# Performance work log

Hardware: AMD Instinct MI355X
Metric: run time of the kernel (lower is better)

## Reference

```python
import jax, jax.numpy as jnp
import numpy as np

WS = 8          # window_size
NH = 8          # num_heads
IQKV = 128      # inner_qk_v_dim
IQKC = 32       # inner_qk_c_dim
IVV = 64        # inner_v_v_dim
EPS = 1e-6
B, HH, WW, DV, DC = 2, 224, 224, 256, 64


def _rmsnorm(x, g):
    return x * jax.lax.rsqrt(jnp.mean(x * x, axis=-1, keepdims=True) + EPS) * g


def _window(x):
    # (b, h, w, d) -> (b, Wh, Ww, ws*ws, d)
    b, h, w, d = x.shape
    x = x.reshape(b, h // WS, WS, w // WS, WS, d).transpose(0, 1, 3, 2, 4, 5)
    return x.reshape(b, h // WS, w // WS, WS * WS, d)


def _unwindow(x, h, w):
    # (b, N, ws*ws, d) -> (b, h, w, d)
    b, _, _, d = x.shape
    x = x.reshape(b, h // WS, w // WS, WS, WS, d).transpose(0, 1, 3, 2, 4, 5)
    return x.reshape(b, h, w, d)


def _source_qkv(V, C, Wqk_v, bqk_v, g_v, Wqk_c, bqk_c, g_c, Wv):
    Vw, Cw = _window(V), _window(C)          # (b, Wh, Ww, n, d)
    b, Wh, Ww, n, _ = Vw.shape
    N = Wh * Ww
    Vavg, Cavg = Vw.mean(-2), Cw.mean(-2)
    qk_v = _rmsnorm(Vavg @ Wqk_v + bqk_v, g_v)   # (b, Wh, Ww, 2*IQKV)
    qk_c = _rmsnorm(Cavg @ Wqk_c + bqk_c, g_c)   # (b, Wh, Ww, 2*IQKC)
    # 'b Wh Ww (H e) -> b H (Wh Ww) e' then chunk2 along e
    qk_v = qk_v.reshape(b, N, NH, -1).transpose(0, 2, 1, 3)
    qk_c = qk_c.reshape(b, N, NH, -1).transpose(0, 2, 1, 3)
    ev, ec = qk_v.shape[-1] // 2, qk_c.shape[-1] // 2
    qv, kv = qk_v[..., :ev], qk_v[..., ev:]
    qc, kc = qk_c[..., :ec], qk_c[..., ec:]
    # value projection: 'b Wh Ww n (e H) -> b H (Wh Ww) (n e)'
    e = IVV // NH
    Vv = (Vw @ Wv).reshape(b, N, n, e, NH).transpose(0, 4, 1, 2, 3).reshape(b, NH, N, n * e)
    return qv, kv, qc, kc, Vv, (Wh, Ww)


def _forward(values0, coords0, values1, coords1,
             Wqk_v, bqk_v, g_v, Wqk_c, bqk_c, g_c, Wv, Wback):
    parts = [_source_qkv(V, C, Wqk_v, bqk_v, g_v, Wqk_c, bqk_c, g_c, Wv)
             for V, C in ((values0, coords0), (values1, coords1))]
    qv = jnp.concatenate([p[0] for p in parts], axis=2)
    kv = jnp.concatenate([p[1] for p in parts], axis=2)
    qc = jnp.concatenate([p[2] for p in parts], axis=2)
    kc = jnp.concatenate([p[3] for p in parts], axis=2)
    Vv = jnp.concatenate([p[4] for p in parts], axis=2)
    scores = (jnp.einsum('bhqe,bhke->bhqk', qv, kv) / jnp.sqrt(jnp.float32(IQKV))
              + jnp.einsum('bhqe,bhke->bhqk', qc, kc) / jnp.sqrt(jnp.float32(IQKC)))
    A = jax.nn.softmax(scores, axis=-1)            # (b, H, N, N)
    rw = jnp.einsum('bhqk,bhkf->bhqf', A, Vv)      # (b, H, N, n*e)
    b, _, N, _ = rw.shape
    n, e = WS * WS, IVV // NH
    # 'b H N (n e) -> b N n (e H)'
    rw = rw.reshape(b, NH, N, n, e).transpose(0, 2, 3, 4, 1).reshape(b, N, n, e * NH)
    rw = rw @ Wback                                # (b, N, n, Dv)
    outs, off = [], 0
    for (V, _), p in zip(((values0, coords0), (values1, coords1)), parts):
        Wh, Ww = p[5]
        Ns = Wh * Ww
        outs.append(_unwindow(rw[:, off:off + Ns], Wh * WS, Ww * WS))
        off += Ns
    return tuple(outs)


def setup_inputs() -> dict:
    key = jax.random.key(0)
    ks = jax.random.split(key, 8)
    s = 0.02
    return {
        'values0': jax.random.normal(ks[0], (B, HH, WW, DV), jnp.float32),
        'coords0': jax.random.normal(ks[1], (B, HH, WW, DC), jnp.float32),
        'values1': jax.random.normal(ks[2], (B, HH, WW, DV), jnp.float32),
        'coords1': jax.random.normal(ks[3], (B, HH, WW, DC), jnp.float32),
        'Wqk_v': s * jax.random.normal(ks[4], (DV, 2 * IQKV), jnp.float32),
        'bqk_v': jnp.zeros((2 * IQKV,), jnp.float32),
        'g_v': jnp.ones((2 * IQKV,), jnp.float32),
        'Wqk_c': s * jax.random.normal(ks[5], (DC, 2 * IQKC), jnp.float32),
        'bqk_c': jnp.zeros((2 * IQKC,), jnp.float32),
        'g_c': jnp.ones((2 * IQKC,), jnp.float32),
        'Wv': s * jax.random.normal(ks[6], (DV, IVV), jnp.float32),
        'Wback': s * jax.random.normal(ks[7], (IVV, DV), jnp.float32),
    }


def reference(values0, coords0, values1, coords1,
              Wqk_v, bqk_v, g_v, Wqk_c, bqk_c, g_c, Wv, Wback):
    return _forward(values0, coords0, values1, coords1,
                    Wqk_v, bqk_v, g_v, Wqk_c, bqk_c, g_c, Wv, Wback)
```

## Files before the change

kernel.cpp:

```cpp
#include <hip/hip_runtime.h>

#define NSRC 784
#define NTOT 1568
#define NHD 8
#define DVC 256
#define DCC 64
#define D20 20
#define FDIM 512
#define OUT_PER_SRC 25690112

typedef short s16x8 __attribute__((ext_vector_type(8)));
typedef unsigned short u16x8 __attribute__((ext_vector_type(8)));
typedef unsigned short u16x4 __attribute__((ext_vector_type(4)));
typedef float f32x4 __attribute__((ext_vector_type(4)));
typedef float f32x16 __attribute__((ext_vector_type(16)));
typedef unsigned u32x4 __attribute__((ext_vector_type(4)));

__device__ __forceinline__ unsigned short f2bf(float x) {
    unsigned u = __float_as_uint(x);
    unsigned r = (u + 0x7FFFu + ((u >> 16) & 1u)) >> 16;
    return (unsigned short)r;
}

__device__ __forceinline__ unsigned cvt_pk_bf16(float lo, float hi) {
    unsigned r;
    asm volatile("v_cvt_pk_bf16_f32 %0, %1, %2" : "=v"(r) : "v"(lo), "v"(hi));
    return r;
}

__device__ __forceinline__ void split_bf(float x, unsigned short& hi, unsigned short& lo) {
    unsigned short h = f2bf(x);
    float hf = __uint_as_float(((unsigned)h) << 16);
    hi = h;
    lo = f2bf(x - hf);
}

__global__ __launch_bounds__(256) void kz_zero(unsigned short* __restrict__ p) {
    size_t i = (size_t)blockIdx.x * 256 + threadIdx.x;
    u16x8 z = (u16x8)0;
    *(u16x8*)&p[i * 8] = z;
}

__global__ __launch_bounds__(256) void k0_wsplit(
    const float* __restrict__ Wv,
    unsigned short* __restrict__ WThi, unsigned short* __restrict__ WTlo) {
    int e = blockIdx.x, dd = threadIdx.x;
    float x = Wv[dd * DCC + e];
    unsigned short h, l;
    split_bf(x, h, l);
    WThi[e * 256 + dd] = h;
    WTlo[e * 256 + dd] = l;
}

__global__ __launch_bounds__(256) void k0b_wback(
    const float* __restrict__ Wb, unsigned short* __restrict__ Wp) {
    int idx = blockIdx.x * 256 + threadIdx.x;
    int jj = idx & 7, lane = (idx >> 3) & 63, hl = (idx >> 9) & 1;
    int kc = (idx >> 10) & 1, mt = idx >> 11;
    int c = mt * 16 + (lane & 15);
    int j = kc * 32 + (lane >> 4) * 8 + jj;
    unsigned short h, l;
    split_bf(Wb[j * 256 + c], h, l);
    Wp[idx] = hl ? l : h;
}

__global__ __launch_bounds__(256) void k1c_avg(
    const float* __restrict__ c0, const float* __restrict__ c1,
    float* __restrict__ Cavg) {
    int wi = blockIdx.x * 4 + (threadIdx.x >> 6);
    int d = threadIdx.x & 63;
    int b = wi / NTOT, N = wi % NTOT;
    int src = N / NSRC, nloc = N % NSRC;
    int wh = nloc / 28, ww = nloc % 28;
    const float* __restrict__ C = src ? c1 : c0;
    int pbase = (b * 224 + wh * 8) * 224 + ww * 8;
    float s = 0.f;
#pragma unroll 8
    for (int p = 0; p < 64; ++p)
        s += C[(size_t)(pbase + (p >> 3) * 224 + (p & 7)) * DCC + d];
    Cavg[(size_t)wi * DCC + d] = s * 0.015625f;
}

__global__ __launch_bounds__(256) void k2_qk(
    const float* __restrict__ Vavg, const float* __restrict__ Cavg,
    const float* __restrict__ Wqkv, const float* __restrict__ bqkv, const float* __restrict__ gv,
    const float* __restrict__ Wqkc, const float* __restrict__ bqkc, const float* __restrict__ gc,
    unsigned short* __restrict__ Qp, unsigned short* __restrict__ Kp) {
    __shared__ float xv[DVC];
    __shared__ float xc[DCC];
    __shared__ float wred[4];
    int blk = blockIdx.x;
    int b = blk / NTOT, N = blk % NTOT;
    int t = threadIdx.x;
    int tile = N >> 5, l31 = N & 31;
    xv[t] = Vavg[(size_t)blk * DVC + t];
    if (t < DCC) xc[t] = Cavg[(size_t)blk * DCC + t];
    __syncthreads();
    float yv = bqkv[t];
#pragma unroll 4
    for (int d = 0; d < DVC; ++d) yv += xv[d] * Wqkv[d * 256 + t];
    float ss = yv * yv;
#pragma unroll
    for (int off = 32; off; off >>= 1) ss += __shfl_xor(ss, off, 64);
    if ((t & 63) == 0) wred[t >> 6] = ss;
    __syncthreads();
    float tot = wred[0] + wred[1] + wred[2] + wred[3];
    float rv = rsqrtf(tot * (1.f / 256.f) + 1e-6f);
    float yn = yv * rv * gv[t];
    int h = t >> 5, c = t & 31;
    int bh = b * NHD + h;
    {
        int isq = (c < 16);
        int d = isq ? c : c - 16;
        float val = isq ? yn * 0.088388347648318447f : yn;
        unsigned short h16, l16;
        split_bf(val, h16, l16);
        int hh = d >> 3, j = d & 7;
        size_t base = ((size_t)(bh * 49 + tile) * 4) * 512 + (size_t)(hh * 32 + l31) * 8 + j;
        unsigned short* dst = isq ? Qp : Kp;
        dst[base] = h16;
        dst[base + 1024] = l16;
    }
    if (t < DCC) {
        float yc = bqkc[t];
#pragma unroll 4
        for (int d = 0; d < DCC; ++d) yc += xc[d] * Wqkc[d * 64 + t];
        float sc = yc * yc;
#pragma unroll
        for (int off = 32; off; off >>= 1) sc += __shfl_xor(sc, off, 64);
        float rc = rsqrtf(sc * (1.f / 64.f) + 1e-6f);
        float ycn = yc * rc * gc[t];
        int h2 = t >> 3, c2 = t & 7;
        int bh2 = b * NHD + h2;
        int isq = (c2 < 4);
        int dd = isq ? c2 : c2 - 4;
        float val = isq ? ycn * 0.17677669529663687f : ycn;
        unsigned short h16, l16;
        split_bf(val, h16, l16);
        size_t base = ((size_t)(bh2 * 49 + tile) * 4 + 1) * 512 + (size_t)l31 * 8 + dd;
        unsigned short* dst = isq ? Qp : Kp;
        dst[base] = h16;
        dst[base + 1024] = l16;
    }
}

__global__ __launch_bounds__(256) void k3_vv(
    const float* __restrict__ v0, const float* __restrict__ v1,
    const unsigned short* __restrict__ WThi, const unsigned short* __restrict__ WTlo,
    unsigned short* __restrict__ Vvb, float* __restrict__ Vavg) {
    __shared__ unsigned short Ahi[64 * 138];
    __shared__ unsigned short Alo[64 * 138];
    int blk = blockIdx.x;
    int b = blk / NTOT, N = blk % NTOT;
    int src = N / NSRC, nloc = N % NSRC;
    int wh = nloc / 28, ww = nloc % 28;
    const float* __restrict__ V = src ? v1 : v0;
    int t = threadIdx.x;
    int w = t >> 6, lane = t & 63;
    int lm = lane & 15, lk = lane >> 4;
    int pxw = w * 16;
    int lhalf = lane >> 5;
    int d4 = (lane & 31) * 4;
    int pbase = (b * 224 + wh * 8) * 224 + ww * 8;

    float ap[8] = {0.f, 0.f, 0.f, 0.f, 0.f, 0.f, 0.f, 0.f};
    f32x4 acc4[4];
#pragma unroll
    for (int nt = 0; nt < 4; ++nt) acc4[nt] = (f32x4)0.f;

#pragma unroll
    for (int ph = 0; ph < 2; ++ph) {
        int d0 = ph * 128;
        float4 xs[8];
#pragma unroll
        for (int i = 0; i < 8; ++i) {
            int px = pxw + i * 2 + lhalf;
            xs[i] = *(const float4*)&V[(size_t)(pbase + (px >> 3) * 224 + (px & 7)) * DVC + d0 + d4];
        }
#pragma unroll
        for (int i = 0; i < 8; ++i) {
            ap[ph * 4 + 0] += xs[i].x; ap[ph * 4 + 1] += xs[i].y;
            ap[ph * 4 + 2] += xs[i].z; ap[ph * 4 + 3] += xs[i].w;
        }
        if (ph) __syncthreads();
#pragma unroll
        for (int i = 0; i < 8; ++i) {
            int px = pxw + i * 2 + lhalf;
            u16x4 h4, l4;
            unsigned short hq, lq;
            split_bf(xs[i].x, hq, lq); h4[0] = hq; l4[0] = lq;
            split_bf(xs[i].y, hq, lq); h4[1] = hq; l4[1] = lq;
            split_bf(xs[i].z, hq, lq); h4[2] = hq; l4[2] = lq;
            split_bf(xs[i].w, hq, lq); h4[3] = hq; l4[3] = lq;
            *(u16x4*)&Ahi[px * 138 + d4] = h4;
            *(u16x4*)&Alo[px * 138 + d4] = l4;
        }
        __syncthreads();
#pragma unroll
        for (int c2 = 0; c2 < 4; ++c2) {
            int dd0 = c2 * 32;
            s16x8 ahi = *(const s16x8*)&Ahi[(pxw + lm) * 138 + dd0 + lk * 8];
            s16x8 alo = *(const s16x8*)&Alo[(pxw + lm) * 138 + dd0 + lk * 8];
#pragma unroll
            for (int nt = 0; nt < 4; ++nt) {
                int e = nt * 16 + lm;
                s16x8 bhi = *(const s16x8*)&WThi[e * 256 + d0 + dd0 + lk * 8];
                s16x8 blo = *(const s16x8*)&WTlo[e * 256 + d0 + dd0 + lk * 8];
                acc4[nt] = __builtin_amdgcn_mfma_f32_16x16x32_bf16(ahi, blo, acc4[nt], 0, 0, 0);
                acc4[nt] = __builtin_amdgcn_mfma_f32_16x16x32_bf16(alo, bhi, acc4[nt], 0, 0, 0);
                acc4[nt] = __builtin_amdgcn_mfma_f32_16x16x32_bf16(ahi, bhi, acc4[nt], 0, 0, 0);
            }
        }
    }
#pragma unroll
    for (int nt = 0; nt < 4; ++nt) {
        int e = nt * 16 + lm;
#pragma unroll
        for (int r = 0; r < 4; ++r) {
            int px = w * 16 + lk * 4 + r;
            Vvb[((size_t)(b * NHD + (e & 7)) * NTOT + N) * FDIM + px * 8 + (e >> 3)] = f2bf(acc4[nt][r]);
        }
    }
#pragma unroll
    for (int j = 0; j < 8; ++j) ap[j] += __shfl_xor(ap[j], 32, 64);
    __syncthreads();
    float* avgb = (float*)Ahi;
    if (lhalf == 0) {
#pragma unroll
        for (int ph = 0; ph < 2; ++ph) {
            float4 v4 = make_float4(ap[ph * 4], ap[ph * 4 + 1], ap[ph * 4 + 2], ap[ph * 4 + 3]);
            *(float4*)&avgb[w * 256 + ph * 128 + d4] = v4;
        }
    }
    __syncthreads();
    Vavg[(size_t)blk * DVC + t] =
        (avgb[t] + avgb[256 + t] + avgb[512 + t] + avgb[768 + t]) * 0.015625f;
}

__global__ __launch_bounds__(256) void k3b_pack(
    const unsigned short* __restrict__ Vvb, unsigned short* __restrict__ Vp) {
    __shared__ unsigned short tile[32 * 520];
    int kt = blockIdx.x, bh = blockIdx.y;
    int t = threadIdx.x;
    const unsigned short* src = Vvb + ((size_t)bh * NTOT + kt * 32) * FDIM;
#pragma unroll
    for (int it = 0; it < 8; ++it) {
        int flat = it * 256 + t;
        int r = flat >> 6, c8 = (flat & 63) * 8;
        *(u16x8*)&tile[r * 520 + c8] = *(const u16x8*)&src[(size_t)r * FDIM + c8];
    }
    __syncthreads();
    unsigned short* dst = Vp + ((size_t)bh * 49 + kt) * 16384;
#pragma unroll
    for (int it = 0; it < 8; ++it) {
        int flato = it * 256 + t;
        int lane = flato & 63;
        int kh = (flato >> 6) & 1;
        int sub = (flato >> 7) & 3;
        int w = flato >> 9;
        int l31 = lane & 31, hh = lane >> 5;
        int f = w * 128 + sub * 32 + l31;
        int kbase = kh * 16 + hh * 8;
        u16x8 v;
#pragma unroll
        for (int j = 0; j < 8; ++j) v[j] = tile[(kbase + j) * 520 + f];
        *(u16x8*)&dst[(size_t)flato * 8] = v;
    }
}

__global__ __launch_bounds__(256) void k4_attn(
    const unsigned short* __restrict__ Qp, const unsigned short* __restrict__ Kp,
    const unsigned short* __restrict__ Vp, float* __restrict__ rw) {
    __shared__ float ebuf[32 * 132];
    int wg = blockIdx.x;
    int qt = wg >> 4, bh = wg & 15;
    int q0 = qt * 32;
    int t = threadIdx.x;
    int w = t >> 6, lane = t & 63;
    int l31 = lane & 31, hh = lane >> 5;

    const unsigned short* __restrict__ Qpb = Qp + ((size_t)(bh * 49 + qt) * 4) * 512 + lane * 8;
    const unsigned short* __restrict__ Kpb = Kp + (size_t)bh * 49 * 2048 + lane * 8;
    const unsigned short* __restrict__ Vpb = Vp + (size_t)bh * 49 * 16384 + lane * 8;

    s16x8 qa0 = *(const s16x8*)&Qpb[0];
    s16x8 qa1 = *(const s16x8*)&Qpb[512];
    s16x8 ql0 = *(const s16x8*)&Qpb[1024];
    s16x8 ql1 = *(const s16x8*)&Qpb[1536];

    s16x8 ka0 = *(const s16x8*)&Kpb[0];
    s16x8 ka1 = *(const s16x8*)&Kpb[512];
    s16x8 kl0 = *(const s16x8*)&Kpb[1024];
    s16x8 kl1 = *(const s16x8*)&Kpb[1536];

    float m = -1e30f, lsum = 0.f;
    f32x16 acc[4];
#pragma unroll
    for (int s = 0; s < 4; ++s) acc[s] = (f32x16)0.f;

    for (int kt = 0; kt < NTOT / 32; ++kt) {
        const unsigned short* Vtile = Vpb + (size_t)kt * 16384 + (w * 8) * 512;
        s16x8 va[8];
#pragma unroll
        for (int fr = 0; fr < 8; ++fr)
            va[fr] = *(const s16x8*)&Vtile[fr * 512];
        int ktn = (kt < 48) ? kt + 1 : 48;
        const unsigned short* Ktn = Kpb + (size_t)ktn * 2048;
        s16x8 kn0 = *(const s16x8*)&Ktn[0];
        s16x8 kn1 = *(const s16x8*)&Ktn[512];
        s16x8 kn2 = *(const s16x8*)&Ktn[1024];
        s16x8 kn3 = *(const s16x8*)&Ktn[1536];

        f32x16 sacc = (f32x16)0.f;
        sacc = __builtin_amdgcn_mfma_f32_32x32x16_bf16(kl0, qa0, sacc, 0, 0, 0);
        sacc = __builtin_amdgcn_mfma_f32_32x32x16_bf16(ka0, ql0, sacc, 0, 0, 0);
        sacc = __builtin_amdgcn_mfma_f32_32x32x16_bf16(ka0, qa0, sacc, 0, 0, 0);
        sacc = __builtin_amdgcn_mfma_f32_32x32x16_bf16(kl1, qa1, sacc, 0, 0, 0);
        sacc = __builtin_amdgcn_mfma_f32_32x32x16_bf16(ka1, ql1, sacc, 0, 0, 0);
        sacc = __builtin_amdgcn_mfma_f32_32x32x16_bf16(ka1, qa1, sacc, 0, 0, 0);

        float tmax = sacc[0];
#pragma unroll
        for (int r = 1; r < 16; ++r) tmax = fmaxf(tmax, sacc[r]);
        tmax = fmaxf(tmax, __shfl_xor(tmax, 32, 64));
        if (__any(tmax > m + 8.f)) {
            float mn = fmaxf(m, tmax);
            float sc = __expf(m - mn);
#pragma unroll
            for (int s = 0; s < 4; ++s) acc[s] = acc[s] * sc;
            lsum *= sc;
            m = mn;
        }
        unsigned P2[8];
        float tsum = 0.f;
#pragma unroll
        for (int j = 0; j < 8; ++j) {
            float pa = __expf(sacc[2 * j] - m);
            float pb = __expf(sacc[2 * j + 1] - m);
            tsum += pa + pb;
            P2[j] = cvt_pk_bf16(pa, pb);
        }
        lsum += tsum + __shfl_xor(tsum, 32, 64);
        unsigned X2[8];
#pragma unroll
        for (int j = 0; j < 8; ++j) X2[j] = (unsigned)__shfl_xor((int)P2[j], 32, 64);
        u32x4 b0u, b1u;
        if (hh == 0) {
            b0u[0] = P2[0]; b0u[1] = P2[1]; b0u[2] = X2[0]; b0u[3] = X2[1];
            b1u[0] = P2[4]; b1u[1] = P2[5]; b1u[2] = X2[4]; b1u[3] = X2[5];
        } else {
            b0u[0] = X2[2]; b0u[1] = X2[3]; b0u[2] = P2[2]; b0u[3] = P2[3];
            b1u[0] = X2[6]; b1u[1] = X2[7]; b1u[2] = P2[6]; b1u[3] = P2[7];
        }
        s16x8 pb0 = __builtin_bit_cast(s16x8, b0u);
        s16x8 pb1 = __builtin_bit_cast(s16x8, b1u);

#pragma unroll
        for (int sub = 0; sub < 4; ++sub) {
            acc[sub] = __builtin_amdgcn_mfma_f32_32x32x16_bf16(va[2 * sub],     pb0, acc[sub], 0, 0, 0);
            acc[sub] = __builtin_amdgcn_mfma_f32_32x32x16_bf16(va[2 * sub + 1], pb1, acc[sub], 0, 0, 0);
        }
        ka0 = kn0; ka1 = kn1; kl0 = kn2; kl1 = kn3;
    }

    float inv = 1.f / lsum;
    float* rwg = rw + ((size_t)bh * NTOT + q0) * FDIM;
#pragma unroll
    for (int c = 0; c < 4; ++c) {
        __syncthreads();
        if (w == c) {
#pragma unroll
            for (int sub = 0; sub < 4; ++sub) {
#pragma unroll
                for (int r = 0; r < 16; ++r) {
                    int fl = sub * 32 + (r & 3) + 8 * (r >> 2) + 4 * hh;
                    ebuf[l31 * 132 + fl] = acc[sub][r] * inv;
                }
            }
        }
        __syncthreads();
        int qr = t >> 3, cb = (t & 7) * 16;
#pragma unroll
        for (int j = 0; j < 4; ++j) {
            *(float4*)&rwg[(size_t)qr * FDIM + c * 128 + cb + j * 4] =
                *(const float4*)&ebuf[qr * 132 + cb + j * 4];
        }
    }
}

__global__ __launch_bounds__(256) void k5_back(
    const float* __restrict__ rw, const unsigned short* __restrict__ Wp,
    float* __restrict__ out) {
    __shared__ unsigned short SB[2 * 64 * 72];
    unsigned short* BhL = SB;
    unsigned short* BlL = SB + 64 * 72;
    int blk = blockIdx.x;
    int b = blk / NTOT, N = blk % NTOT;
    int src = N / NSRC, nloc = N % NSRC;
    int wh = nloc / 28, ww = nloc % 28;
    int t = threadIdx.x;
    int w = t >> 6, lane = t & 63;
    int lm = lane & 15, lk = lane >> 4;
    int pbase = (b * 224 + wh * 8) * 224 + ww * 8;

#pragma unroll
    for (int i = 0; i < 4; ++i) {
        int flat4 = i * 256 + t;
        int h = flat4 >> 7;
        int f0 = (flat4 & 127) * 4;
        float4 v = *(const float4*)&rw[((size_t)(b * NHD + h) * NTOT + N) * FDIM + f0];
        int n = f0 >> 3;
        int ebase = f0 & 7;
        float vv[4] = {v.x, v.y, v.z, v.w};
#pragma unroll
        for (int u = 0; u < 4; ++u) {
            int j8 = ebase + u;
            unsigned short h16, l16;
            split_bf(vv[u], h16, l16);
            int col = ((j8 ^ (n & 7)) << 3) | h;
            BhL[n * 72 + col] = h16;
            BlL[n * 72 + col] = l16;
        }
    }
    __syncthreads();

    f32x4 acc[4][4];
#pragma unroll
    for (int mi = 0; mi < 4; ++mi)
#pragma unroll
        for (int nt = 0; nt < 4; ++nt) acc[mi][nt] = (f32x4)0.f;

    const unsigned short* Wpw = Wp + (size_t)(w * 4) * 2048 + lane * 8;
#pragma unroll
    for (int kc = 0; kc < 2; ++kc) {
        s16x8 Ah[4], Al[4], Bh4[4], Bl4[4];
#pragma unroll
        for (int mi = 0; mi < 4; ++mi) {
            int base = mi * 2048 + kc * 1024;
            Ah[mi] = *(const s16x8*)&Wpw[base];
            Al[mi] = *(const s16x8*)&Wpw[base + 512];
        }
#pragma unroll
        for (int nt = 0; nt < 4; ++nt) {
            int n = nt * 16 + lm;
            int addr = n * 72 + (((kc * 4 + lk) ^ (n & 7)) << 3);
            Bh4[nt] = *(const s16x8*)&BhL[addr];
            Bl4[nt] = *(const s16x8*)&BlL[addr];
        }
#pragma unroll
        for (int mi = 0; mi < 4; ++mi)
#pragma unroll
            for (int nt = 0; nt < 4; ++nt) {
                acc[mi][nt] = __builtin_amdgcn_mfma_f32_16x16x32_bf16(Ah[mi], Bl4[nt], acc[mi][nt], 0, 0, 0);
                acc[mi][nt] = __builtin_amdgcn_mfma_f32_16x16x32_bf16(Al[mi], Bh4[nt], acc[mi][nt], 0, 0, 0);
                acc[mi][nt] = __builtin_amdgcn_mfma_f32_16x16x32_bf16(Ah[mi], Bh4[nt], acc[mi][nt], 0, 0, 0);
            }
    }

    float* eb = (float*)SB;
    float* outp = out + (size_t)src * OUT_PER_SRC;
#pragma unroll
    for (int ch = 0; ch < 4; ++ch) {
        __syncthreads();
        if (w == ch) {
#pragma unroll
            for (int mi = 0; mi < 4; ++mi)
#pragma unroll
                for (int nt = 0; nt < 4; ++nt)
#pragma unroll
                    for (int r = 0; r < 4; ++r) {
                        int n = nt * 16 + lm;
                        int cl = mi * 16 + lk * 4 + r;
                        eb[n * 68 + cl] = acc[mi][nt][r];
                    }
        }
        __syncthreads();
#pragma unroll
        for (int i = 0; i < 4; ++i) {
            int fl4 = i * 256 + t;
            int n = fl4 >> 4, c4 = (fl4 & 15) * 4;
            int opix = pbase + (n >> 3) * 224 + (n & 7);
            *(float4*)&outp[(size_t)opix * DVC + ch * 64 + c4] =
                *(const float4*)&eb[n * 68 + c4];
        }
    }
}

extern "C" void kernel_launch(void* const* d_in, const int* in_sizes, int n_in,
                              void* d_out, int out_size, void* d_ws, size_t ws_size,
                              hipStream_t stream) {
    const float* v0   = (const float*)d_in[0];
    const float* c0   = (const float*)d_in[1];
    const float* v1   = (const float*)d_in[2];
    const float* c1   = (const float*)d_in[3];
    const float* Wqkv = (const float*)d_in[4];
    const float* bqkv = (const float*)d_in[5];
    const float* gv   = (const float*)d_in[6];
    const float* Wqkc = (const float*)d_in[7];
    const float* bqkc = (const float*)d_in[8];
    const float* gc   = (const float*)d_in[9];
    const float* Wv   = (const float*)d_in[10];
    const float* Wbk  = (const float*)d_in[11];

    float* ws = (float*)d_ws;
    float* rw   = ws;
    float* Vavg = ws;
    float* Cavg = ws + 802816;
    unsigned short* Qp   = (unsigned short*)(ws + 12845056);
    unsigned short* Kp   = (unsigned short*)(ws + 13647872);
    unsigned short* WThi = (unsigned short*)(ws + 14450688);
    unsigned short* WTlo = (unsigned short*)(ws + 14458880);
    unsigned short* Vvb  = (unsigned short*)(ws + 14467072);
    unsigned short* Vp   = (unsigned short*)(ws + 20889600);
    unsigned short* Wp   = (unsigned short*)(ws + 27312128);

    float* outp = (float*)d_out;

    kz_zero  <<<1568, 256, 0, stream>>>(Qp);
    k0_wsplit<<<64, 256, 0, stream>>>(Wv, WThi, WTlo);
    k0b_wback<<<256, 256, 0, stream>>>(Wbk, Wp);
    k3_vv    <<<2 * NTOT, 256, 0, stream>>>(v0, v1, WThi, WTlo, Vvb, Vavg);
    k1c_avg  <<<784, 256, 0, stream>>>(c0, c1, Cavg);
    k2_qk    <<<2 * NTOT, 256, 0, stream>>>(Vavg, Cavg, Wqkv, bqkv, gv, Wqkc, bqkc, gc, Qp, Kp);
    k3b_pack <<<dim3(49, 16), 256, 0, stream>>>(Vvb, Vp);
    k4_attn  <<<784, 256, 0, stream>>>(Qp, Kp, Vp, rw);
    k5_back  <<<2 * NTOT, 256, 0, stream>>>(rw, Wp, outp);
}
```

Baseline: 389.9 us.

## Swizzle k3_vv LDS tile, stage output through LDS for coalesced Vvb writes

In k3_vv the padded LDS tile is replaced by an XOR-swizzled 128-wide layout to avoid bank conflicts, and the B-operand loads are hoisted ahead of the MFMA loop. The MFMA results are now transposed through LDS and written to Vvb as contiguous 16-byte vectors per block, replacing the scattered 2-byte global stores. k3b_pack's read indexing is changed to match the new intermediate layout. The cost is an extra LDS round-trip and barrier, plus a more complex gather in the pack kernel.

```diff
diff --git a/kernel.cpp b/kernel.cpp
--- a/kernel.cpp
+++ b/kernel.cpp
@@ -148,8 +148,8 @@
     const float* __restrict__ v0, const float* __restrict__ v1,
     const unsigned short* __restrict__ WThi, const unsigned short* __restrict__ WTlo,
     unsigned short* __restrict__ Vvb, float* __restrict__ Vavg) {
-    __shared__ unsigned short Ahi[64 * 138];
-    __shared__ unsigned short Alo[64 * 138];
+    __shared__ unsigned short Ahi[64 * 128];
+    __shared__ unsigned short Alo[64 * 128];
     int blk = blockIdx.x;
     int b = blk / NTOT, N = blk % NTOT;
     int src = N / NSRC, nloc = N % NSRC;
@@ -192,39 +192,47 @@
             split_bf(xs[i].y, hq, lq); h4[1] = hq; l4[1] = lq;
             split_bf(xs[i].z, hq, lq); h4[2] = hq; l4[2] = lq;
             split_bf(xs[i].w, hq, lq); h4[3] = hq; l4[3] = lq;
-            *(u16x4*)&Ahi[px * 138 + d4] = h4;
-            *(u16x4*)&Alo[px * 138 + d4] = l4;
+            int addr = px * 128 + (((d4 >> 3) ^ (px & 7)) << 3) + (d4 & 7);
+            *(u16x4*)&Ahi[addr] = h4;
+            *(u16x4*)&Alo[addr] = l4;
         }
         __syncthreads();
 #pragma unroll
         for (int c2 = 0; c2 < 4; ++c2) {
             int dd0 = c2 * 32;
-            s16x8 ahi = *(const s16x8*)&Ahi[(pxw + lm) * 138 + dd0 + lk * 8];
-            s16x8 alo = *(const s16x8*)&Alo[(pxw + lm) * 138 + dd0 + lk * 8];
+            s16x8 Bh4[4], Bl4[4];
 #pragma unroll
             for (int nt = 0; nt < 4; ++nt) {
                 int e = nt * 16 + lm;
-                s16x8 bhi = *(const s16x8*)&WThi[e * 256 + d0 + dd0 + lk * 8];
-                s16x8 blo = *(const s16x8*)&WTlo[e * 256 + d0 + dd0 + lk * 8];
-                acc4[nt] = __builtin_amdgcn_mfma_f32_16x16x32_bf16(ahi, blo, acc4[nt], 0, 0, 0);
-                acc4[nt] = __builtin_amdgcn_mfma_f32_16x16x32_bf16(alo, bhi, acc4[nt], 0, 0, 0);
-                acc4[nt] = __builtin_amdgcn_mfma_f32_16x16x32_bf16(ahi, bhi, acc4[nt], 0, 0, 0);
+                Bh4[nt] = *(const s16x8*)&WThi[e * 256 + d0 + dd0 + lk * 8];
+                Bl4[nt] = *(const s16x8*)&WTlo[e * 256 + d0 + dd0 + lk * 8];
             }
-        }
-    }
+            int row = pxw + lm;
+            int raddr = row * 128 + ((((dd0 >> 3) + lk) ^ (row & 7)) << 3);
+            s16x8 ahi = *(const s16x8*)&Ahi[raddr];
+            s16x8 alo = *(const s16x8*)&Alo[raddr];
+#pragma unroll
+            for (int nt = 0; nt < 4; ++nt) {
+                acc4[nt] = __builtin_amdgcn_mfma_f32_16x16x32_bf16(ahi, Bl4[nt], acc4[nt], 0, 0, 0);
+                acc4[nt] = __builtin_amdgcn_mfma_f32_16x16x32_bf16(alo, Bh4[nt], acc4[nt], 0, 0, 0);
+                acc4[nt] = __builtin_amdgcn_mfma_f32_16x16x32_bf16(ahi, Bh4[nt], acc4[nt], 0, 0, 0);
+            }
+        }
+    }
+    __syncthreads();
+    unsigned short* eb = Ahi;
 #pragma unroll
     for (int nt = 0; nt < 4; ++nt) {
         int e = nt * 16 + lm;
 #pragma unroll
         for (int r = 0; r < 4; ++r) {
-            int px = w * 16 + lk * 4 + r;
-            Vvb[((size_t)(b * NHD + (e & 7)) * NTOT + N) * FDIM + px * 8 + (e >> 3)] = f2bf(acc4[nt][r]);
+            int px = pxw + lk * 4 + r;
+            eb[px * 66 + e] = f2bf(acc4[nt][r]);
         }
     }
 #pragma unroll
     for (int j = 0; j < 8; ++j) ap[j] += __shfl_xor(ap[j], 32, 64);
-    __syncthreads();
-    float* avgb = (float*)Ahi;
+    float* avgb = (float*)Alo;
     if (lhalf == 0) {
 #pragma unroll
         for (int ph = 0; ph < 2; ++ph) {
@@ -233,21 +241,37 @@
         }
     }
     __syncthreads();
+    unsigned short* dst = Vvb + (size_t)blk * 4096;
+#pragma unroll
+    for (int i = 0; i < 2; ++i) {
+        int flat16 = i * 256 + t;
+        int f3 = flat16 >> 6;
+        int h = (flat16 >> 3) & 7;
+        int px8 = (flat16 & 7) * 8;
+        u16x8 vv;
+#pragma unroll
+        for (int u = 0; u < 8; ++u) vv[u] = eb[(px8 + u) * 66 + f3 * 8 + h];
+        *(u16x8*)&dst[flat16 * 8] = vv;
+    }
     Vavg[(size_t)blk * DVC + t] =
         (avgb[t] + avgb[256 + t] + avgb[512 + t] + avgb[768 + t]) * 0.015625f;
 }
 
 __global__ __launch_bounds__(256) void k3b_pack(
     const unsigned short* __restrict__ Vvb, unsigned short* __restrict__ Vp) {
-    __shared__ unsigned short tile[32 * 520];
+    __shared__ unsigned short tile[32 * 576];
     int kt = blockIdx.x, bh = blockIdx.y;
+    int b = bh >> 3, h = bh & 7;
     int t = threadIdx.x;
-    const unsigned short* src = Vvb + ((size_t)bh * NTOT + kt * 32) * FDIM;
 #pragma unroll
     for (int it = 0; it < 8; ++it) {
         int flat = it * 256 + t;
-        int r = flat >> 6, c8 = (flat & 63) * 8;
-        *(u16x8*)&tile[r * 520 + c8] = *(const u16x8*)&src[(size_t)r * FDIM + c8];
+        int r5 = flat >> 6;
+        int c = flat & 63;
+        int f3 = c >> 3, px8 = (c & 7) * 8;
+        const unsigned short* s =
+            Vvb + ((size_t)(b * NTOT + kt * 32 + r5) * 8 + f3) * 512 + h * 64 + px8;
+        *(u16x8*)&tile[r5 * 576 + f3 * 72 + px8] = *(const u16x8*)s;
     }
     __syncthreads();
     unsigned short* dst = Vp + ((size_t)bh * 49 + kt) * 16384;
@@ -263,7 +287,8 @@
         int kbase = kh * 16 + hh * 8;
         u16x8 v;
 #pragma unroll
-        for (int j = 0; j < 8; ++j) v[j] = tile[(kbase + j) * 520 + f];
+        for (int j = 0; j < 8; ++j)
+            v[j] = tile[(kbase + j) * 576 + (f & 7) * 72 + (f >> 3)];
         *(u16x8*)&dst[(size_t)flato * 8] = v;
     }
 }
```

Result: faster. 359.0 us (-7.9%).
